# Performance work log

Measured on AMD Instinct MI355X. Metric: run time of the kernel, lower is better.

The kernel has to match this reference:

```python
import jax, jax.numpy as jnp
import numpy as np

B, H, KVH, S, D = 2, 32, 8, 2048, 128
NEG = jnp.float32(-1e9)


def _causal_mask(b, s):
    # additive causal mask [b, 1, s, s]: 0 where allowed, -1e9 where masked
    tri = jnp.tril(jnp.ones((s, s), dtype=bool))
    m = jnp.where(tri, jnp.float32(0.0), NEG)
    return jnp.broadcast_to(m[None, None], (b, 1, s, s))


def setup_inputs() -> dict:
    key = jax.random.key(0)
    k1, k2, k3 = jax.random.split(key, 3)
    return {
        "query": jax.random.normal(k1, (B, H, S, D), dtype=jnp.float32),
        "key": jax.random.normal(k2, (B, KVH, S, D), dtype=jnp.float32),
        "value": jax.random.normal(k3, (B, S, KVH, D), dtype=jnp.float32),  # pre-permute layout
        "attention_mask": _causal_mask(B, S),
        "scale_attn": jnp.float32(np.sqrt(D)),
        "num_key_value_groups": H // KVH,
    }


def reference(query, key, value, attention_mask, scale_attn, num_key_value_groups):
    # llama branch of _IPEXScaleDotProductRef.forward (no layer_past, no head_mask)
    value = jnp.transpose(value, (0, 2, 1, 3))  # [b, kvh, s, d]
    present = (key, value)
    # _repeat_kv == repeat_interleave along head dim
    k = jnp.repeat(key, num_key_value_groups, axis=1)    # [b, h, s, d]
    v = jnp.repeat(value, num_key_value_groups, axis=1)  # [b, h, s, d]
    attn_weights = jnp.einsum("bhqd,bhkd->bhqk", query, k) / scale_attn
    attn_weights = attn_weights + attention_mask
    attn_weights = jax.nn.softmax(attn_weights.astype(jnp.float32), axis=-1).astype(query.dtype)
    attn_output = jnp.einsum("bhqk,bhkd->bhqd", attn_weights, v)
    return attn_output, attn_weights, present
```

## Files before the change

kernel.cpp:

```cpp
#include <hip/hip_runtime.h>

#define BB 2
#define HH 32
#define KVHH 8
#define SS 2048
#define DD 128
#define GG 4
#define BHT (BB*HH)
#define TILES (SS/64)

#define O_OFF  ((size_t)0)
#define W_OFF  ((size_t)BB*HH*SS*DD)
#define PK_OFF (W_OFF + (size_t)BB*HH*SS*SS)
#define PV_OFF (PK_OFF + (size_t)BB*KVHH*SS*DD)

#define QS_STRIDE 132
#define ES_STRIDE 68

__global__ __launch_bounds__(256) void pass1(
    const float* __restrict__ q, const float* __restrict__ k,
    const float* __restrict__ v, const float* __restrict__ scale_p,
    float* __restrict__ out)
{
  __shared__ __align__(16) float q_s[64*QS_STRIDE];
  __shared__ __align__(16) float kv_s[64*QS_STRIDE];
  __shared__ __align__(16) float e_s[64*ES_STRIDE];

  const int bh   = blockIdx.x;
  const int tile = blockIdx.y;
  const int i0   = tile * 64;
  const int b    = bh / HH;
  const int h    = bh % HH;
  const int kvh  = h / GG;
  const int tid  = threadIdx.x;
  const int tx   = tid & 15, ty = tid >> 4;

  const float inv_scale = 1.0f / scale_p[0];

  {
    const float4* qg = (const float4*)(q + ((size_t)bh*SS + i0)*DD);
    #pragma unroll
    for (int it = 0; it < 8; ++it) {
      int f = tid + 256*it;
      int r = f >> 5, c4 = f & 31;
      float4 val = qg[(size_t)r*32 + c4];
      float* dst = &q_s[r*QS_STRIDE + c4*4];
      dst[0]=val.x; dst[1]=val.y; dst[2]=val.z; dst[3]=val.w;
    }
  }

  float o_acc[4][8];
  #pragma unroll
  for (int a=0;a<4;++a)
    #pragma unroll
    for (int c=0;c<8;++c) o_acc[a][c]=0.f;

  const float* kg_base = k + ((size_t)(b*KVHH + kvh)*SS)*DD;
  const float* vg_base = v + ((size_t)b*SS*KVHH + (size_t)kvh)*DD;
  float* w_out = out + W_OFF + (size_t)bh*SS*SS;

  for (int j0 = 0; j0 <= i0; j0 += 64) {
    __syncthreads();
    #pragma unroll
    for (int it = 0; it < 8; ++it) {
      int f = tid + 256*it;
      int r = f >> 5, c4 = f & 31;
      const float4* src = (const float4*)(kg_base + (size_t)(j0 + r)*DD);
      float4 val = src[c4];
      float* dst = &kv_s[r*QS_STRIDE + c4*4];
      dst[0]=val.x; dst[1]=val.y; dst[2]=val.z; dst[3]=val.w;
    }
    __syncthreads();
    float acc[4][4];
    #pragma unroll
    for (int a=0;a<4;++a)
      #pragma unroll
      for(int c=0;c<4;++c) acc[a][c]=0.f;
    for (int k4 = 0; k4 < DD; k4 += 4) {
      float4 av[4], bv[4];
      #pragma unroll
      for (int rr=0;rr<4;++rr) av[rr] = *(const float4*)&q_s[(ty+16*rr)*QS_STRIDE + k4];
      #pragma unroll
      for (int cc=0;cc<4;++cc) bv[cc] = *(const float4*)&kv_s[(tx+16*cc)*QS_STRIDE + k4];
      #pragma unroll
      for (int rr=0;rr<4;++rr)
        #pragma unroll
        for (int cc=0;cc<4;++cc)
          acc[rr][cc] += av[rr].x*bv[cc].x + av[rr].y*bv[cc].y
                       + av[rr].z*bv[cc].z + av[rr].w*bv[cc].w;
    }
    #pragma unroll
    for (int rr=0;rr<4;++rr) {
      int i_row = i0 + ty + 16*rr;
      #pragma unroll
      for (int cc=0;cc<4;++cc) {
        int j_col = j0 + tx + 16*cc;
        float e = (j_col <= i_row) ? __expf(acc[rr][cc]*inv_scale) : 0.f;
        e_s[(ty+16*rr)*ES_STRIDE + (tx+16*cc)] = e;
        w_out[(size_t)i_row*SS + j_col] = e;
      }
    }
    __syncthreads();
    #pragma unroll
    for (int it = 0; it < 8; ++it) {
      int f = tid + 256*it;
      int r = f >> 5, c4 = f & 31;
      const float4* src = (const float4*)(vg_base + (size_t)(j0 + r)*KVHH*DD);
      float4 val = src[c4];
      float* dst = &kv_s[r*QS_STRIDE + c4*4];
      dst[0]=val.x; dst[1]=val.y; dst[2]=val.z; dst[3]=val.w;
    }
    __syncthreads();
    for (int j4 = 0; j4 < 64; j4 += 4) {
      float4 e4[4];
      #pragma unroll
      for (int rr=0;rr<4;++rr) e4[rr] = *(const float4*)&e_s[(ty+16*rr)*ES_STRIDE + j4];
      #pragma unroll
      for (int jj=0;jj<4;++jj) {
        float vv[8];
        #pragma unroll
        for (int c2=0;c2<8;++c2) vv[c2] = kv_s[(j4+jj)*QS_STRIDE + tx + 16*c2];
        #pragma unroll
        for (int rr=0;rr<4;++rr) {
          float ev = (jj==0)?e4[rr].x:(jj==1)?e4[rr].y:(jj==2)?e4[rr].z:e4[rr].w;
          #pragma unroll
          for (int c2=0;c2<8;++c2) o_acc[rr][c2] += ev * vv[c2];
        }
      }
    }
  }
  float* o_out = out + O_OFF + ((size_t)bh*SS + i0)*DD;
  #pragma unroll
  for (int rr=0;rr<4;++rr)
    #pragma unroll
    for (int c2=0;c2<8;++c2)
      o_out[(size_t)(ty+16*rr)*DD + tx + 16*c2] = o_acc[rr][c2];
}

__global__ __launch_bounds__(256) void pass2(float* __restrict__ out, float* __restrict__ ws_inv)
{
  const int row = blockIdx.x;
  const int i   = row & (SS-1);
  float* w = out + W_OFF + (size_t)row*SS;
  const int tid = threadIdx.x;
  float vals[8];
  float s = 0.f;
  #pragma unroll
  for (int it=0; it<8; ++it) {
    int j = tid + 256*it;
    float x = (j <= i) ? w[j] : 0.f;
    vals[it] = x; s += x;
  }
  #pragma unroll
  for (int off=32; off>0; off>>=1) s += __shfl_down(s, off, 64);
  __shared__ float part[4];
  __shared__ float tot;
  if ((tid & 63)==0) part[tid>>6] = s;
  __syncthreads();
  if (tid==0) {
    float t = part[0]+part[1]+part[2]+part[3];
    float inv = 1.0f / t;
    ws_inv[row] = inv;
    tot = inv;
  }
  __syncthreads();
  float inv = tot;
  #pragma unroll
  for (int it=0;it<8;++it) {
    int j = tid + 256*it;
    w[j] = (j <= i) ? vals[it]*inv : 0.f;
  }
}

__global__ __launch_bounds__(256) void pass3(float* __restrict__ out, const float* __restrict__ ws_inv)
{
  size_t idx = (size_t)blockIdx.x*256 + threadIdx.x;
  int row = (int)(idx >> 7);
  out[O_OFF + idx] *= ws_inv[row];
}

__global__ __launch_bounds__(256) void pass4(const float* __restrict__ k, const float* __restrict__ v,
                                             float* __restrict__ out)
{
  const size_t NK = (size_t)BB*KVHH*SS*DD/4;
  size_t t = (size_t)blockIdx.x*256 + threadIdx.x;
  if (t < NK) {
    ((float4*)(out + PK_OFF))[t] = ((const float4*)k)[t];
  } else {
    size_t u = t - NK;
    int c4 = (int)(u & 31);
    size_t rrow = u >> 5;
    int s_  = (int)(rrow & (SS-1));
    size_t bk = rrow >> 11;
    int kvh = (int)(bk & (KVHH-1));
    int b_  = (int)(bk >> 3);
    size_t src = ((size_t)(b_*SS + s_)*KVHH + kvh)*32 + c4;
    ((float4*)(out + PV_OFF))[u] = ((const float4*)v)[src];
  }
}

extern "C" void kernel_launch(void* const* d_in, const int* in_sizes, int n_in,
                              void* d_out, int out_size, void* d_ws, size_t ws_size,
                              hipStream_t stream) {
  (void)in_sizes; (void)n_in; (void)out_size; (void)ws_size;
  const float* q = (const float*)d_in[0];
  const float* k = (const float*)d_in[1];
  const float* v = (const float*)d_in[2];
  const float* scale = (const float*)d_in[4];
  float* out = (float*)d_out;
  float* ws  = (float*)d_ws;

  pass1<<<dim3(BHT, TILES), 256, 0, stream>>>(q, k, v, scale, out);
  pass2<<<BB*HH*SS, 256, 0, stream>>>(out, ws);
  pass3<<<(BB*HH*SS*DD)/256, 256, 0, stream>>>(out, ws);
  pass4<<<(2*BB*KVHH*SS*DD/4)/256, 256, 0, stream>>>(k, v, out);
}
```

Before: 2.926 ms.

## Fuse row-sum and output normalization into attention pass, swizzle LDS, nontemporal I/O

New measurement: 2.821 ms. 3.6% less time.

```diff
diff --git a/kernel.cpp b/kernel.cpp
--- a/kernel.cpp
+++ b/kernel.cpp
@@ -1,4 +1,6 @@
 #include <hip/hip_runtime.h>
+
+typedef float v4f __attribute__((ext_vector_type(4)));
 
 #define BB 2
 #define HH 32
@@ -8,29 +10,29 @@
 #define GG 4
 #define BHT (BB*HH)
 #define TILES (SS/64)
+#define NWG (BHT*TILES)
 
 #define O_OFF  ((size_t)0)
 #define W_OFF  ((size_t)BB*HH*SS*DD)
 #define PK_OFF (W_OFF + (size_t)BB*HH*SS*SS)
 #define PV_OFF (PK_OFF + (size_t)BB*KVHH*SS*DD)
 
-#define QS_STRIDE 132
-#define ES_STRIDE 68
-
-__global__ __launch_bounds__(256) void pass1(
+__global__ __launch_bounds__(256, 2) void pass1(
     const float* __restrict__ q, const float* __restrict__ k,
     const float* __restrict__ v, const float* __restrict__ scale_p,
-    float* __restrict__ out)
+    float* __restrict__ out, float* __restrict__ ws_inv)
 {
-  __shared__ __align__(16) float q_s[64*QS_STRIDE];
-  __shared__ __align__(16) float kv_s[64*QS_STRIDE];
-  __shared__ __align__(16) float e_s[64*ES_STRIDE];
-
-  const int bh   = blockIdx.x;
-  const int tile = blockIdx.y;
+  __shared__ v4f q_s4[64*32];
+  __shared__ v4f kv_s4[64*32];
+  __shared__ float e_s[64*64];
+
+  const int bid = blockIdx.x;
+  const int logical = ((bid & 7) << 8) | (bid >> 3);
+  const int bh   = logical >> 5;
+  const int tile = logical & 31;
   const int i0   = tile * 64;
   const int b    = bh / HH;
-  const int h    = bh % HH;
+  const int h    = bh - b*HH;
   const int kvh  = h / GG;
   const int tid  = threadIdx.x;
   const int tx   = tid & 15, ty = tid >> 4;
@@ -38,14 +40,12 @@
   const float inv_scale = 1.0f / scale_p[0];
 
   {
-    const float4* qg = (const float4*)(q + ((size_t)bh*SS + i0)*DD);
+    const v4f* qg = (const v4f*)(q + ((size_t)bh*SS + i0)*DD);
     #pragma unroll
     for (int it = 0; it < 8; ++it) {
       int f = tid + 256*it;
       int r = f >> 5, c4 = f & 31;
-      float4 val = qg[(size_t)r*32 + c4];
-      float* dst = &q_s[r*QS_STRIDE + c4*4];
-      dst[0]=val.x; dst[1]=val.y; dst[2]=val.z; dst[3]=val.w;
+      q_s4[r*32 + (c4 ^ (r & 31))] = __builtin_nontemporal_load(&qg[(size_t)r*32 + c4]);
     }
   }
 
@@ -54,6 +54,7 @@
   for (int a=0;a<4;++a)
     #pragma unroll
     for (int c=0;c<8;++c) o_acc[a][c]=0.f;
+  float rs[4] = {0.f, 0.f, 0.f, 0.f};
 
   const float* kg_base = k + ((size_t)(b*KVHH + kvh)*SS)*DD;
   const float* vg_base = v + ((size_t)b*SS*KVHH + (size_t)kvh)*DD;
@@ -65,10 +66,8 @@
     for (int it = 0; it < 8; ++it) {
       int f = tid + 256*it;
       int r = f >> 5, c4 = f & 31;
-      const float4* src = (const float4*)(kg_base + (size_t)(j0 + r)*DD);
-      float4 val = src[c4];
-      float* dst = &kv_s[r*QS_STRIDE + c4*4];
-      dst[0]=val.x; dst[1]=val.y; dst[2]=val.z; dst[3]=val.w;
+      const v4f* src = (const v4f*)(kg_base + (size_t)(j0 + r)*DD);
+      kv_s4[r*32 + (c4 ^ (r & 31))] = src[c4];
     }
     __syncthreads();
     float acc[4][4];
@@ -76,12 +75,19 @@
     for (int a=0;a<4;++a)
       #pragma unroll
       for(int c=0;c<4;++c) acc[a][c]=0.f;
-    for (int k4 = 0; k4 < DD; k4 += 4) {
-      float4 av[4], bv[4];
-      #pragma unroll
-      for (int rr=0;rr<4;++rr) av[rr] = *(const float4*)&q_s[(ty+16*rr)*QS_STRIDE + k4];
-      #pragma unroll
-      for (int cc=0;cc<4;++cc) bv[cc] = *(const float4*)&kv_s[(tx+16*cc)*QS_STRIDE + k4];
+    #pragma unroll 4
+    for (int k4 = 0; k4 < 32; ++k4) {
+      v4f av[4], bv[4];
+      #pragma unroll
+      for (int rr=0;rr<4;++rr) {
+        int row = ty + 16*rr;
+        av[rr] = q_s4[row*32 + (k4 ^ (row & 31))];
+      }
+      #pragma unroll
+      for (int cc=0;cc<4;++cc) {
+        int row = tx + 16*cc;
+        bv[cc] = kv_s4[row*32 + (k4 ^ (row & 31))];
+      }
       #pragma unroll
       for (int rr=0;rr<4;++rr)
         #pragma unroll
@@ -96,8 +102,8 @@
       for (int cc=0;cc<4;++cc) {
         int j_col = j0 + tx + 16*cc;
         float e = (j_col <= i_row) ? __expf(acc[rr][cc]*inv_scale) : 0.f;
-        e_s[(ty+16*rr)*ES_STRIDE + (tx+16*cc)] = e;
-        w_out[(size_t)i_row*SS + j_col] = e;
+        e_s[(ty+16*rr)*64 + tx + 16*cc] = e;
+        rs[rr] += e;
       }
     }
     __syncthreads();
@@ -105,78 +111,82 @@
     for (int it = 0; it < 8; ++it) {
       int f = tid + 256*it;
       int r = f >> 5, c4 = f & 31;
-      const float4* src = (const float4*)(vg_base + (size_t)(j0 + r)*KVHH*DD);
-      float4 val = src[c4];
-      float* dst = &kv_s[r*QS_STRIDE + c4*4];
-      dst[0]=val.x; dst[1]=val.y; dst[2]=val.z; dst[3]=val.w;
-    }
-    __syncthreads();
+      const v4f* src = (const v4f*)(vg_base + (size_t)(j0 + r)*KVHH*DD);
+      kv_s4[r*32 + (c4 ^ (r & 31))] = src[c4];
+    }
+    {
+      float* wb = w_out + (size_t)i0*SS + j0;
+      #pragma unroll
+      for (int it = 0; it < 4; ++it) {
+        int f = tid + 256*it;
+        int r = f >> 4, c4 = f & 15;
+        v4f val = *(const v4f*)&e_s[r*64 + c4*4];
+        __builtin_nontemporal_store(val, (v4f*)(wb + (size_t)r*SS) + c4);
+      }
+    }
+    __syncthreads();
+    #pragma unroll 2
     for (int j4 = 0; j4 < 64; j4 += 4) {
-      float4 e4[4];
-      #pragma unroll
-      for (int rr=0;rr<4;++rr) e4[rr] = *(const float4*)&e_s[(ty+16*rr)*ES_STRIDE + j4];
+      v4f e4[4];
+      #pragma unroll
+      for (int rr=0;rr<4;++rr) e4[rr] = *(const v4f*)&e_s[(ty+16*rr)*64 + j4];
       #pragma unroll
       for (int jj=0;jj<4;++jj) {
-        float vv[8];
-        #pragma unroll
-        for (int c2=0;c2<8;++c2) vv[c2] = kv_s[(j4+jj)*QS_STRIDE + tx + 16*c2];
+        int vr = (j4+jj) & 31;
+        v4f v0 = kv_s4[(j4+jj)*32 + (tx ^ vr)];
+        v4f v1 = kv_s4[(j4+jj)*32 + ((tx+16) ^ vr)];
         #pragma unroll
         for (int rr=0;rr<4;++rr) {
           float ev = (jj==0)?e4[rr].x:(jj==1)?e4[rr].y:(jj==2)?e4[rr].z:e4[rr].w;
-          #pragma unroll
-          for (int c2=0;c2<8;++c2) o_acc[rr][c2] += ev * vv[c2];
+          o_acc[rr][0] += ev*v0.x; o_acc[rr][1] += ev*v0.y;
+          o_acc[rr][2] += ev*v0.z; o_acc[rr][3] += ev*v0.w;
+          o_acc[rr][4] += ev*v1.x; o_acc[rr][5] += ev*v1.y;
+          o_acc[rr][6] += ev*v1.z; o_acc[rr][7] += ev*v1.w;
         }
       }
     }
   }
-  float* o_out = out + O_OFF + ((size_t)bh*SS + i0)*DD;
+
   #pragma unroll
-  for (int rr=0;rr<4;++rr)
-    #pragma unroll
-    for (int c2=0;c2<8;++c2)
-      o_out[(size_t)(ty+16*rr)*DD + tx + 16*c2] = o_acc[rr][c2];
-}
-
-__global__ __launch_bounds__(256) void pass2(float* __restrict__ out, float* __restrict__ ws_inv)
+  for (int off=1; off<16; off<<=1)
+    #pragma unroll
+    for (int rr=0;rr<4;++rr) rs[rr] += __shfl_xor(rs[rr], off);
+
+  float* o_base = out + O_OFF + ((size_t)bh*SS + i0)*DD;
+  #pragma unroll
+  for (int rr=0;rr<4;++rr) {
+    float invr = 1.0f / rs[rr];
+    if (tx == 0) ws_inv[(size_t)bh*SS + i0 + ty + 16*rr] = invr;
+    v4f w0, w1;
+    w0.x=o_acc[rr][0]*invr; w0.y=o_acc[rr][1]*invr; w0.z=o_acc[rr][2]*invr; w0.w=o_acc[rr][3]*invr;
+    w1.x=o_acc[rr][4]*invr; w1.y=o_acc[rr][5]*invr; w1.z=o_acc[rr][6]*invr; w1.w=o_acc[rr][7]*invr;
+    float* orow = o_base + (size_t)(ty+16*rr)*DD;
+    __builtin_nontemporal_store(w0, (v4f*)orow + tx);
+    __builtin_nontemporal_store(w1, (v4f*)orow + 16 + tx);
+  }
+}
+
+__global__ __launch_bounds__(256) void pass2(float* __restrict__ out, const float* __restrict__ ws_inv)
 {
-  const int row = blockIdx.x;
-  const int i   = row & (SS-1);
-  float* w = out + W_OFF + (size_t)row*SS;
-  const int tid = threadIdx.x;
-  float vals[8];
-  float s = 0.f;
-  #pragma unroll
-  for (int it=0; it<8; ++it) {
-    int j = tid + 256*it;
-    float x = (j <= i) ? w[j] : 0.f;
-    vals[it] = x; s += x;
-  }
-  #pragma unroll
-  for (int off=32; off>0; off>>=1) s += __shfl_down(s, off, 64);
-  __shared__ float part[4];
-  __shared__ float tot;
-  if ((tid & 63)==0) part[tid>>6] = s;
-  __syncthreads();
-  if (tid==0) {
-    float t = part[0]+part[1]+part[2]+part[3];
-    float inv = 1.0f / t;
-    ws_inv[row] = inv;
-    tot = inv;
-  }
-  __syncthreads();
-  float inv = tot;
-  #pragma unroll
-  for (int it=0;it<8;++it) {
-    int j = tid + 256*it;
-    w[j] = (j <= i) ? vals[it]*inv : 0.f;
-  }
-}
-
-__global__ __launch_bounds__(256) void pass3(float* __restrict__ out, const float* __restrict__ ws_inv)
-{
-  size_t idx = (size_t)blockIdx.x*256 + threadIdx.x;
-  int row = (int)(idx >> 7);
-  out[O_OFF + idx] *= ws_inv[row];
+  v4f* w = (v4f*)(out + W_OFF);
+  size_t base = (size_t)blockIdx.x * (size_t)(256*32) + threadIdx.x;
+  #pragma unroll 4
+  for (int it = 0; it < 32; ++it) {
+    size_t idx = base + (size_t)(256*it);
+    int row = (int)(idx >> 9);
+    int i   = row & (SS-1);
+    int j0  = ((int)idx & 511) << 2;
+    v4f x = {0.f, 0.f, 0.f, 0.f};
+    if (j0 <= i) {
+      float inv = ws_inv[row];
+      v4f vv = __builtin_nontemporal_load(&w[idx]);
+      x.x = vv.x*inv;
+      x.y = (j0+1 <= i) ? vv.y*inv : 0.f;
+      x.z = (j0+2 <= i) ? vv.z*inv : 0.f;
+      x.w = (j0+3 <= i) ? vv.w*inv : 0.f;
+    }
+    __builtin_nontemporal_store(x, &w[idx]);
+  }
 }
 
 __global__ __launch_bounds__(256) void pass4(const float* __restrict__ k, const float* __restrict__ v,
@@ -185,7 +195,8 @@
   const size_t NK = (size_t)BB*KVHH*SS*DD/4;
   size_t t = (size_t)blockIdx.x*256 + threadIdx.x;
   if (t < NK) {
-    ((float4*)(out + PK_OFF))[t] = ((const float4*)k)[t];
+    v4f val = __builtin_nontemporal_load(((const v4f*)k) + t);
+    __builtin_nontemporal_store(val, (v4f*)(out + PK_OFF) + t);
   } else {
     size_t u = t - NK;
     int c4 = (int)(u & 31);
@@ -195,7 +206,8 @@
     int kvh = (int)(bk & (KVHH-1));
     int b_  = (int)(bk >> 3);
     size_t src = ((size_t)(b_*SS + s_)*KVHH + kvh)*32 + c4;
-    ((float4*)(out + PV_OFF))[u] = ((const float4*)v)[src];
+    v4f val = __builtin_nontemporal_load(((const v4f*)v) + src);
+    __builtin_nontemporal_store(val, (v4f*)(out + PV_OFF) + u);
   }
 }
 
@@ -210,8 +222,7 @@
   float* out = (float*)d_out;
   float* ws  = (float*)d_ws;
 
-  pass1<<<dim3(BHT, TILES), 256, 0, stream>>>(q, k, v, scale, out);
-  pass2<<<BB*HH*SS, 256, 0, stream>>>(out, ws);
-  pass3<<<(BB*HH*SS*DD)/256, 256, 0, stream>>>(out, ws);
+  pass1<<<NWG, 256, 0, stream>>>(q, k, v, scale, out, ws);
+  pass2<<<8192, 256, 0, stream>>>(out, ws);
   pass4<<<(2*BB*KVHH*SS*DD/4)/256, 256, 0, stream>>>(k, v, out);
 }
```
